# Performance work log

Measured on AMD Instinct MI355X. Metric: run time of the kernel, lower is better.

Reference implementation:

```python
import jax, jax.numpy as jnp
import numpy as np

# config: nsql-350M-like, 8 layers
L, D, H, HD, FF, V, RD, MP = 8, 1024, 16, 64, 4096, 51200, 32, 4


def setup_inputs() -> dict:
    key = jax.random.key(0)
    ks = jax.random.split(key, 8)
    B, S = 1, 1024
    s = 0.02
    return {
        'idx': jax.random.randint(ks[0], (B, S), 0, V),
        'input_pos': jnp.arange(S),
        'emb': jax.random.normal(ks[1], (V, D)) * s,
        'Wqkv': jax.random.normal(ks[2], (L, 3 * D, D)) * s,
        'Wo': jax.random.normal(ks[3], (L, D, D)) * s,
        'ln1_w': jnp.ones((L, D)), 'ln1_b': jnp.zeros((L, D)),
        'fc_in_w': jax.random.normal(ks[4], (L, FF, D)) * s,
        'fc_in_b': jnp.zeros((L, FF)),
        'fc_out_w': jax.random.normal(ks[5], (L, D, FF)) * s,
        'fc_out_b': jnp.zeros((L, D)),
        'lnf_w': jnp.ones((D,)), 'lnf_b': jnp.zeros((D,)),
        'lm_w': jax.random.normal(ks[6], (V, D)) * s,
        'lm_b': jnp.zeros((V,)),
    }


def _layer_norm(x, w, b, eps=1e-5):
    mu = jnp.mean(x, axis=-1, keepdims=True)
    var = jnp.var(x, axis=-1, keepdims=True)
    return (x - mu) * jax.lax.rsqrt(var + eps) * w + b


def _new_gelu(x):
    # transformers NewGELUActivation == tanh-approx gelu
    return jax.nn.gelu(x, approximate=True)


def _sincos(input_pos):
    # create_sinusoidal_positions over rotary_dim, gathered at input_pos
    inv_freq = 1.0 / (10000.0 ** (jnp.arange(0, RD, 2, dtype=jnp.float32) / RD))
    ang = input_pos.astype(jnp.float32)[:, None] * inv_freq          # [S, RD/2]
    # repeat_interleave(..., 2, dim=-1) -> interleaved sin/cos, shape [1,S,1,RD]
    sin = jnp.repeat(jnp.sin(ang), 2, axis=-1)[None, :, None, :]
    cos = jnp.repeat(jnp.cos(ang), 2, axis=-1)[None, :, None, :]
    return sin, cos


def _rotary(x, sin, cos):
    # x: [B,S,H,HD]; GPT-J interleaved rotary on first RD dims
    xr, xp = x[..., :RD], x[..., RD:]
    x1, x2 = xr[..., ::2], xr[..., 1::2]
    rot = jnp.stack((-x2, x1), axis=-1).reshape(xr.shape)  # rotate_every_two
    return jnp.concatenate([xr * cos + rot * sin, xp], axis=-1)


def reference(idx, input_pos, emb, Wqkv, Wo, ln1_w, ln1_b, fc_in_w, fc_in_b,
              fc_out_w, fc_out_b, lnf_w, lnf_b, lm_w, lm_b):
    B, S = idx.shape
    x = emb[idx]                                        # [B,S,D]
    sin, cos = _sincos(input_pos)
    causal = jnp.tril(jnp.ones((S, S), dtype=bool))
    neg = jnp.finfo(x.dtype).min
    ld = D // MP

    def split_heads(t):
        # CodeGen _split_heads with mp_num=4: [B,S,MP,ld] -> [B,S,H,HD]
        return t.reshape(B, S, MP, H // MP, HD).reshape(B, S, H, HD)

    for l in range(L):
        h = _layer_norm(x, ln1_w[l], ln1_b[l])
        qkv = (h @ Wqkv[l].T).reshape(B, S, MP, 3 * ld)
        q, v, k = qkv[..., :ld], qkv[..., ld:2 * ld], qkv[..., 2 * ld:]  # q,v,k order!
        q = _rotary(split_heads(q), sin, cos)
        k = _rotary(split_heads(k), sin, cos)
        vh = split_heads(v)
        q, k, vh = (jnp.transpose(t, (0, 2, 1, 3)) for t in (q, k, vh))  # [B,H,S,HD]
        scores = jnp.einsum('bhqd,bhkd->bhqk', q, k) / jnp.sqrt(jnp.asarray(HD, x.dtype))
        scores = jnp.where(causal, scores, neg)
        att = jax.nn.softmax(scores, axis=-1)
        y = jnp.einsum('bhqk,bhkd->bhqd', att, vh)
        y = jnp.transpose(y, (0, 2, 1, 3)).reshape(B, S, D)
        attn_out = y @ Wo[l].T
        mlp = _new_gelu(h @ fc_in_w[l].T + fc_in_b[l]) @ fc_out_w[l].T + fc_out_b[l]
        x = attn_out + mlp + x                          # parallel block + residual

    x = _layer_norm(x, lnf_w, lnf_b)
    return x @ lm_w.T + lm_b                            # [B,S,V]
```

## Files before the change

kernel.cpp:

```cpp
#include <hip/hip_runtime.h>

#define SQ 1024
#define DIM 1024
#define NH 16
#define HDIM 64
#define FFD 4096
#define NV 51200
#define NL 8
#define LDBUF 5120

typedef __bf16 bf16x8 __attribute__((ext_vector_type(8)));
typedef float f32x4 __attribute__((ext_vector_type(4)));

__device__ __forceinline__ unsigned short f2bf(float f) {
    union { float f; unsigned int i; } v; v.f = f;
    unsigned int r = v.i + 0x7fffu + ((v.i >> 16) & 1u);
    return (unsigned short)(r >> 16);
}
__device__ __forceinline__ float gelu_tanh(float x) {
    float x3 = x * x * x;
    return 0.5f * x * (1.0f + tanhf(0.79788456080286535588f * (x + 0.044715f * x3)));
}

#define GLD16(gp, lp) __builtin_amdgcn_global_load_lds( \
    (__attribute__((address_space(1))) void*)(gp), \
    (__attribute__((address_space(3))) void*)(lp), 16, 0, 0)
#define VMCNT0 asm volatile("s_waitcnt vmcnt(0)" ::: "memory")

__global__ void cvt4_kernel(const float* __restrict__ w0, const float* __restrict__ w1,
                            const float* __restrict__ w2, const float* __restrict__ w3,
                            unsigned short* __restrict__ d0, unsigned short* __restrict__ d1,
                            unsigned short* __restrict__ d2, unsigned short* __restrict__ d3) {
    const int b = blockIdx.x;
    const float* s; unsigned short* d; long off;
    if (b < 1536)      { s = w0; d = d0; off = (long)b * 2048; }
    else if (b < 2048) { s = w1; d = d1; off = (long)(b - 1536) * 2048; }
    else if (b < 4096) { s = w2; d = d2; off = (long)(b - 2048) * 2048; }
    else               { s = w3; d = d3; off = (long)(b - 4096) * 2048; }
    const long i = off + threadIdx.x * 8;
    float4 a = *reinterpret_cast<const float4*>(s + i);
    float4 c = *reinterpret_cast<const float4*>(s + i + 4);
    bf16x8 w;
    w[0] = (__bf16)a.x; w[1] = (__bf16)a.y; w[2] = (__bf16)a.z; w[3] = (__bf16)a.w;
    w[4] = (__bf16)c.x; w[5] = (__bf16)c.y; w[6] = (__bf16)c.z; w[7] = (__bf16)c.w;
    *reinterpret_cast<bf16x8*>(d + i) = w;
}
__global__ void cvt_kernel(const float* __restrict__ src, unsigned short* __restrict__ dst) {
    const long i = ((long)blockIdx.x * 256 + threadIdx.x) * 8;
    float4 a = *reinterpret_cast<const float4*>(src + i);
    float4 b = *reinterpret_cast<const float4*>(src + i + 4);
    bf16x8 w;
    w[0] = (__bf16)a.x; w[1] = (__bf16)a.y; w[2] = (__bf16)a.z; w[3] = (__bf16)a.w;
    w[4] = (__bf16)b.x; w[5] = (__bf16)b.y; w[6] = (__bf16)b.z; w[7] = (__bf16)b.w;
    *reinterpret_cast<bf16x8*>(dst + i) = w;
}

__global__ void sincos_kernel(const int* __restrict__ pos, float2* __restrict__ sc) {
    const int t = blockIdx.x * 256 + threadIdx.x;
    if (t >= SQ * 16) return;
    const int s = t >> 4, i = t & 15;
    const float ang = (float)pos[s] * powf(10000.0f, -(float)i / 16.0f);
    sc[t] = make_float2(sinf(ang), cosf(ang));
}

__global__ void embed_kernel(const int* __restrict__ idx, const float* __restrict__ emb,
                             float* __restrict__ x) {
    const int s = blockIdx.x;
    const int d = threadIdx.x * 4;
    const int row = idx[s];
    *reinterpret_cast<float4*>(x + (long)s * DIM + d) =
        *reinterpret_cast<const float4*>(emb + (long)row * DIM + d);
}

template <bool RED>
__global__ __launch_bounds__(256) void ln_kernel(float* __restrict__ x,
                                                 const float* __restrict__ part,
                                                 const float* __restrict__ w,
                                                 const float* __restrict__ b,
                                                 unsigned short* __restrict__ out) {
    __shared__ float red[8];
    const int s = blockIdx.x, tid = threadIdx.x;
    const long fidx = (long)s * 256 + tid;
    float4 v = reinterpret_cast<const float4*>(x)[fidx];
    if (RED) {
        #pragma unroll
        for (int z = 0; z < 8; z++) {
            float4 p = reinterpret_cast<const float4*>(part + (long)z * SQ * DIM)[fidx];
            v.x += p.x; v.y += p.y; v.z += p.z; v.w += p.w;
        }
        reinterpret_cast<float4*>(x)[fidx] = v;
    }
    float sum = v.x + v.y + v.z + v.w;
    float sq = v.x * v.x + v.y * v.y + v.z * v.z + v.w * v.w;
    #pragma unroll
    for (int off = 32; off; off >>= 1) { sum += __shfl_xor(sum, off); sq += __shfl_xor(sq, off); }
    const int wid = tid >> 6, lane = tid & 63;
    if (lane == 0) { red[wid * 2] = sum; red[wid * 2 + 1] = sq; }
    __syncthreads();
    sum = red[0] + red[2] + red[4] + red[6];
    sq  = red[1] + red[3] + red[5] + red[7];
    const float mu = sum * (1.0f / DIM);
    const float var = sq * (1.0f / DIM) - mu * mu;
    const float rstd = rsqrtf(var + 1e-5f);
    const int d = tid * 4;
    float vv[4] = {v.x, v.y, v.z, v.w};
    ushort4 o;
    unsigned short* op = (unsigned short*)&o;
    #pragma unroll
    for (int j = 0; j < 4; j++)
        op[j] = f2bf((vv[j] - mu) * rstd * w[d + j] + b[d + j]);
    *reinterpret_cast<ushort4*>(out + (long)s * DIM + d) = o;
}

__global__ __launch_bounds__(256) void gemm_qkv_fcin(const unsigned short* __restrict__ A,
                                                     const unsigned short* __restrict__ B1,
                                                     const unsigned short* __restrict__ B2,
                                                     const float* __restrict__ bias,
                                                     unsigned short* __restrict__ ffout,
                                                     const float2* __restrict__ sc,
                                                     unsigned short* __restrict__ qt,
                                                     unsigned short* __restrict__ kt,
                                                     unsigned short* __restrict__ vt) {
    __shared__ __align__(16) unsigned short As[2][128 * 64];
    __shared__ __align__(16) unsigned short Bs[2][128 * 64];
    const int tid = threadIdx.x;
    const int nwg = gridDim.x, qch = nwg >> 3;
    const int sb = (blockIdx.x & 7) * qch + (blockIdx.x >> 3);
    const int mb = sb & 7, nb = sb >> 3;
    const int m0 = mb * 128, n0 = nb * 128;
    const int lane = tid & 63, wid = tid >> 6;
    const int l15 = lane & 15, lhi = lane >> 4;
    const int wr = wid >> 1, wc = wid & 1;
    const int sw = l15 & 7;

    const unsigned short* Bbase = B1;
    int nloc = n0;
    if (nb >= 24) { Bbase = B2; nloc = n0 - 3072; }

    f32x4 acc[4][4];
    #pragma unroll
    for (int i = 0; i < 4; i++)
        #pragma unroll
        for (int j = 0; j < 4; j++) acc[i][j] = (f32x4){0.f, 0.f, 0.f, 0.f};

    const int wbase = (tid & ~63) * 8;

    auto stage = [&](int buf, int kt_) {
        const int k0 = kt_ << 6;
        #pragma unroll
        for (int i = 0; i < 4; i++) {
            const int e = (i * 256 + tid) * 8;
            const int r = e >> 6;
            const int cs = (((e >> 3) & 7) ^ (r & 7)) * 8;
            GLD16(A + (long)(m0 + r) * DIM + k0 + cs, &As[buf][i * 2048 + wbase]);
        }
        #pragma unroll
        for (int i = 0; i < 4; i++) {
            const int e = (i * 256 + tid) * 8;
            const int r = e >> 6;
            const int cs = (((e >> 3) & 7) ^ (r & 7)) * 8;
            GLD16(Bbase + (long)(nloc + r) * 1024 + k0 + cs, &Bs[buf][i * 2048 + wbase]);
        }
    };
    auto compute = [&](int buf) {
        #pragma unroll
        for (int ks = 0; ks < 2; ks++) {
            bf16x8 af[4], bfr[4];
            #pragma unroll
            for (int mf = 0; mf < 4; mf++)
                af[mf] = *reinterpret_cast<const bf16x8*>(
                    &As[buf][(wr * 64 + mf * 16 + l15) * 64 + ((ks * 4 + lhi) ^ sw) * 8]);
            #pragma unroll
            for (int nf = 0; nf < 4; nf++)
                bfr[nf] = *reinterpret_cast<const bf16x8*>(
                    &Bs[buf][(wc * 64 + nf * 16 + l15) * 64 + ((ks * 4 + lhi) ^ sw) * 8]);
            #pragma unroll
            for (int mf = 0; mf < 4; mf++)
                #pragma unroll
                for (int nf = 0; nf < 4; nf++)
                    acc[mf][nf] = __builtin_amdgcn_mfma_f32_16x16x32_bf16(af[mf], bfr[nf], acc[mf][nf], 0, 0, 0);
        }
    };

    int cur = 0;
    stage(0, 0);
    VMCNT0; __syncthreads();
    for (int kt_ = 0; kt_ < 16; kt_++) {
        if (kt_ + 1 < 16) stage(cur ^ 1, kt_ + 1);
        compute(cur);
        if (kt_ + 1 < 16) { VMCNT0; __syncthreads(); cur ^= 1; }
    }

    if (nb < 24) {
        #pragma unroll
        for (int nf = 0; nf < 4; nf++) {
            const int col = n0 + wc * 64 + nf * 16 + l15;
            const int g = col / 768;
            const int r768 = col - g * 768;
            const int sec = r768 >> 8;
            const int off = r768 & 255;
            const int h = g * 4 + (off >> 6);
            const int d = off & 63;
            const bool isrot = (d < 32);
            const int dodd = d & 1;
            #pragma unroll
            for (int mf = 0; mf < 4; mf++) {
                #pragma unroll
                for (int j = 0; j < 4; j++) {
                    const int row = m0 + wr * 64 + mf * 16 + lhi * 4 + j;
                    float v = acc[mf][nf][j];
                    const float pv = __shfl_xor(v, 1);
                    float outv = v;
                    if (isrot && sec != 1) {
                        const float2 scv = sc[row * 16 + (d >> 1)];
                        outv = dodd ? (v * scv.y + pv * scv.x)
                                    : (v * scv.y - pv * scv.x);
                    }
                    if (sec == 0)      qt[((long)(h * SQ + row)) * HDIM + d] = f2bf(outv);
                    else if (sec == 2) kt[((long)(h * SQ + row)) * HDIM + d] = f2bf(outv);
                    else               vt[(long)h * (HDIM * SQ) + (long)d * SQ + row] = f2bf(outv);
                }
            }
        }
    } else {
        #pragma unroll
        for (int nf = 0; nf < 4; nf++) {
            const int col = n0 + wc * 64 + nf * 16 + l15;
            #pragma unroll
            for (int mf = 0; mf < 4; mf++) {
                #pragma unroll
                for (int j = 0; j < 4; j++) {
                    const int row = m0 + wr * 64 + mf * 16 + lhi * 4 + j;
                    float v = gelu_tanh(acc[mf][nf][j] + bias[col - 3072]);
                    ffout[(long)row * LDBUF + (col - 3072)] = f2bf(v);
                }
            }
        }
    }
}

__global__ __launch_bounds__(256) void attn_fcout(const unsigned short* __restrict__ qt,
                                                  const unsigned short* __restrict__ kt,
                                                  const unsigned short* __restrict__ vt,
                                                  unsigned short* __restrict__ buf,
                                                  const unsigned short* __restrict__ fcw,
                                                  const float* __restrict__ fcb,
                                                  float* __restrict__ parts) {
    __shared__ __align__(16) unsigned short smem[32768];
    const int tid = threadIdx.x, lane = tid & 63, wid = tid >> 6;
    const int l15 = lane & 15, lhi = lane >> 4;
    const int sw = l15 & 7;
    const int wbase = (tid & ~63) * 8;

    if (blockIdx.x < 256) {
        unsigned short* Ks0 = smem;
        unsigned short* Vs0 = smem + 8192;
        unsigned short* Psw = smem + 16384 + wid * 1024;
        const int h = blockIdx.x & 15;
        const int qb = 15 - ((int)blockIdx.x >> 4);
        const int q0 = qb * 64 + wid * 16;

        bf16x8 aq[2];
        {
            const unsigned short* qp = qt + ((long)(h * SQ + q0 + l15)) * HDIM;
            aq[0] = *reinterpret_cast<const bf16x8*>(qp + lhi * 8);
            aq[1] = *reinterpret_cast<const bf16x8*>(qp + 32 + lhi * 8);
        }
        f32x4 o[4];
        #pragma unroll
        for (int nf = 0; nf < 4; nf++) o[nf] = (f32x4){0.f, 0.f, 0.f, 0.f};
        float mrow[4] = {-1e30f, -1e30f, -1e30f, -1e30f};
        float lrow[4] = {0.f, 0.f, 0.f, 0.f};

        auto stageKV = [&](int b, int kv0) {
            #pragma unroll
            for (int i = 0; i < 2; i++) {
                const int e = (i * 256 + tid) * 8;
                const int r = e >> 6;
                const int cs = (((e >> 3) & 7) ^ (r & 7)) * 8;
                GLD16(kt + ((long)(h * SQ + kv0 + r)) * HDIM + cs, Ks0 + b * 4096 + i * 2048 + wbase);
                GLD16(vt + (long)h * (HDIM * SQ) + (long)r * SQ + kv0 + cs, Vs0 + b * 4096 + i * 2048 + wbase);
            }
        };

        int cur = 0;
        stageKV(0, 0);
        VMCNT0; __syncthreads();
        for (int kvt = 0; kvt <= qb; kvt++) {
            const int kv0 = kvt * 64;
            if (kvt < qb) stageKV(cur ^ 1, kv0 + 64);

            f32x4 sa[4];
            #pragma unroll
            for (int hc = 0; hc < 4; hc++) sa[hc] = (f32x4){0.f, 0.f, 0.f, 0.f};
            #pragma unroll
            for (int hc = 0; hc < 4; hc++)
                #pragma unroll
                for (int ks = 0; ks < 2; ks++) {
                    bf16x8 bk = *reinterpret_cast<const bf16x8*>(
                        Ks0 + cur * 4096 + (hc * 16 + l15) * 64 + ((ks * 4 + lhi) ^ sw) * 8);
                    sa[hc] = __builtin_amdgcn_mfma_f32_16x16x32_bf16(aq[ks], bk, sa[hc], 0, 0, 0);
                }
            float pr[4][4], mb[4];
            #pragma unroll
            for (int j = 0; j < 4; j++) {
                const int qi = q0 + lhi * 4 + j;
                #pragma unroll
                for (int hc = 0; hc < 4; hc++) {
                    const int ki = kv0 + hc * 16 + l15;
                    const float sv = sa[hc][j] * 0.125f;
                    pr[hc][j] = (ki <= qi) ? sv : -1e30f;
                }
                mb[j] = fmaxf(fmaxf(pr[0][j], pr[1][j]), fmaxf(pr[2][j], pr[3][j]));
            }
            #pragma unroll
            for (int off = 1; off < 16; off <<= 1)
                #pragma unroll
                for (int j = 0; j < 4; j++) mb[j] = fmaxf(mb[j], __shfl_xor(mb[j], off));
            float alpha[4], psum[4];
            #pragma unroll
            for (int j = 0; j < 4; j++) {
                const float mn = fmaxf(mrow[j], mb[j]);
                alpha[j] = __expf(mrow[j] - mn);
                mrow[j] = mn;
                psum[j] = 0.f;
                #pragma unroll
                for (int hc = 0; hc < 4; hc++) { pr[hc][j] = __expf(pr[hc][j] - mn); psum[j] += pr[hc][j]; }
            }
            #pragma unroll
            for (int off = 1; off < 16; off <<= 1)
                #pragma unroll
                for (int j = 0; j < 4; j++) psum[j] += __shfl_xor(psum[j], off);
            #pragma unroll
            for (int j = 0; j < 4; j++) lrow[j] = lrow[j] * alpha[j] + psum[j];
            #pragma unroll
            for (int nf = 0; nf < 4; nf++)
                #pragma unroll
                for (int j = 0; j < 4; j++) o[nf][j] *= alpha[j];
            #pragma unroll
            for (int hc = 0; hc < 4; hc++)
                #pragma unroll
                for (int j = 0; j < 4; j++) {
                    const int prow = lhi * 4 + j;
                    const int pc8 = (hc * 2 + (l15 >> 3)) ^ (prow & 7);
                    Psw[prow * 64 + pc8 * 8 + (l15 & 7)] = f2bf(pr[hc][j]);
                }
            bf16x8 ap[2];
            ap[0] = *reinterpret_cast<const bf16x8*>(Psw + l15 * 64 + ((0 + lhi) ^ sw) * 8);
            ap[1] = *reinterpret_cast<const bf16x8*>(Psw + l15 * 64 + ((4 + lhi) ^ sw) * 8);
            #pragma unroll
            for (int nf = 0; nf < 4; nf++)
                #pragma unroll
                for (int ks2 = 0; ks2 < 2; ks2++) {
                    bf16x8 bv = *reinterpret_cast<const bf16x8*>(
                        Vs0 + cur * 4096 + (nf * 16 + l15) * 64 + ((ks2 * 4 + lhi) ^ sw) * 8);
                    o[nf] = __builtin_amdgcn_mfma_f32_16x16x32_bf16(ap[ks2], bv, o[nf], 0, 0, 0);
                }
            if (kvt < qb) { VMCNT0; __syncthreads(); cur ^= 1; }
        }
        #pragma unroll
        for (int nf = 0; nf < 4; nf++)
            #pragma unroll
            for (int j = 0; j < 4; j++) {
                const int row = q0 + lhi * 4 + j;
                buf[(long)row * LDBUF + h * HDIM + nf * 16 + l15] = f2bf(o[nf][j] / lrow[j]);
            }
    } else {
        unsigned short* As0 = smem;
        unsigned short* Bs0 = smem + 16384;
        const int b2 = (int)blockIdx.x - 256;
        const int sb = (b2 & 7) * 64 + (b2 >> 3);
        const int kz = sb & 7, nb = (sb >> 3) & 7, mb = sb >> 6;
        const int m0 = mb * 128, n0 = nb * 128;
        const int kt0 = kz * 8;
        const int wr = wid >> 1, wc = wid & 1;
        const unsigned short* Aff = buf + DIM;

        f32x4 acc[4][4];
        #pragma unroll
        for (int i = 0; i < 4; i++)
            #pragma unroll
            for (int j = 0; j < 4; j++) acc[i][j] = (f32x4){0.f, 0.f, 0.f, 0.f};

        auto stage = [&](int bf_, int kt_) {
            const int k0 = kt_ << 6;
            #pragma unroll
            for (int i = 0; i < 4; i++) {
                const int e = (i * 256 + tid) * 8;
                const int r = e >> 6;
                const int cs = (((e >> 3) & 7) ^ (r & 7)) * 8;
                GLD16(Aff + (long)(m0 + r) * LDBUF + k0 + cs, As0 + bf_ * 8192 + i * 2048 + wbase);
                GLD16(fcw + (long)(n0 + r) * FFD + k0 + cs, Bs0 + bf_ * 8192 + i * 2048 + wbase);
            }
        };
        auto compute = [&](int bf_) {
            #pragma unroll
            for (int ks = 0; ks < 2; ks++) {
                bf16x8 af[4], bfr[4];
                #pragma unroll
                for (int mf = 0; mf < 4; mf++)
                    af[mf] = *reinterpret_cast<const bf16x8*>(
                        As0 + bf_ * 8192 + (wr * 64 + mf * 16 + l15) * 64 + ((ks * 4 + lhi) ^ sw) * 8);
                #pragma unroll
                for (int nf = 0; nf < 4; nf++)
                    bfr[nf] = *reinterpret_cast<const bf16x8*>(
                        Bs0 + bf_ * 8192 + (wc * 64 + nf * 16 + l15) * 64 + ((ks * 4 + lhi) ^ sw) * 8);
                #pragma unroll
                for (int mf = 0; mf < 4; mf++)
                    #pragma unroll
                    for (int nf = 0; nf < 4; nf++)
                        acc[mf][nf] = __builtin_amdgcn_mfma_f32_16x16x32_bf16(af[mf], bfr[nf], acc[mf][nf], 0, 0, 0);
            }
        };

        int cur = 0;
        stage(0, kt0);
        VMCNT0; __syncthreads();
        for (int t = 0; t < 8; t++) {
            if (t + 1 < 8) stage(cur ^ 1, kt0 + t + 1);
            compute(cur);
            if (t + 1 < 8) { VMCNT0; __syncthreads(); cur ^= 1; }
        }

        float* P = parts + (long)kz * SQ * DIM;
        #pragma unroll
        for (int nf = 0; nf < 4; nf++) {
            const int col = n0 + wc * 64 + nf * 16 + l15;
            const float bv = (kz == 0) ? fcb[col] : 0.f;
            #pragma unroll
            for (int mf = 0; mf < 4; mf++) {
                #pragma unroll
                for (int j = 0; j < 4; j++) {
                    const int row = m0 + wr * 64 + mf * 16 + lhi * 4 + j;
                    P[(long)row * DIM + col] = acc[mf][nf][j] + bv;
                }
            }
        }
    }
}

__global__ __launch_bounds__(256) void wo_rmw(const unsigned short* __restrict__ buf,
                                              const unsigned short* __restrict__ wo,
                                              float* __restrict__ parts) {
    __shared__ __align__(16) unsigned short As[2][128 * 64];
    __shared__ __align__(16) unsigned short Bs[2][128 * 64];
    const int tid = threadIdx.x;
    const int sb = (blockIdx.x & 7) * 32 + (blockIdx.x >> 3);
    const int kz = sb & 3, nb = (sb >> 2) & 7, mb = sb >> 5;
    const int m0 = mb * 128, n0 = nb * 128;
    const int kt0 = kz * 4;
    const int lane = tid & 63, wid = tid >> 6;
    const int l15 = lane & 15, lhi = lane >> 4;
    const int wr = wid >> 1, wc = wid & 1;
    const int sw = l15 & 7;
    const int wbase = (tid & ~63) * 8;

    f32x4 acc[4][4];
    #pragma unroll
    for (int i = 0; i < 4; i++)
        #pragma unroll
        for (int j = 0; j < 4; j++) acc[i][j] = (f32x4){0.f, 0.f, 0.f, 0.f};

    auto stage = [&](int bf_, int kt_) {
        const int k0 = kt_ << 6;
        #pragma unroll
        for (int i = 0; i < 4; i++) {
            const int e = (i * 256 + tid) * 8;
            const int r = e >> 6;
            const int cs = (((e >> 3) & 7) ^ (r & 7)) * 8;
            GLD16(buf + (long)(m0 + r) * LDBUF + k0 + cs, &As[bf_][i * 2048 + wbase]);
            GLD16(wo + (long)(n0 + r) * DIM + k0 + cs, &Bs[bf_][i * 2048 + wbase]);
        }
    };
    auto compute = [&](int bf_) {
        #pragma unroll
        for (int ks = 0; ks < 2; ks++) {
            bf16x8 af[4], bfr[4];
            #pragma unroll
            for (int mf = 0; mf < 4; mf++)
                af[mf] = *reinterpret_cast<const bf16x8*>(
                    &As[bf_][(wr * 64 + mf * 16 + l15) * 64 + ((ks * 4 + lhi) ^ sw) * 8]);
            #pragma unroll
            for (int nf = 0; nf < 4; nf++)
                bfr[nf] = *reinterpret_cast<const bf16x8*>(
                    &Bs[bf_][(wc * 64 + nf * 16 + l15) * 64 + ((ks * 4 + lhi) ^ sw) * 8]);
            #pragma unroll
            for (int mf = 0; mf < 4; mf++)
                #pragma unroll
                for (int nf = 0; nf < 4; nf++)
                    acc[mf][nf] = __builtin_amdgcn_mfma_f32_16x16x32_bf16(af[mf], bfr[nf], acc[mf][nf], 0, 0, 0);
        }
    };

    int cur = 0;
    stage(0, kt0);
    VMCNT0; __syncthreads();
    for (int t = 0; t < 4; t++) {
        if (t + 1 < 4) stage(cur ^ 1, kt0 + t + 1);
        compute(cur);
        if (t + 1 < 4) { VMCNT0; __syncthreads(); cur ^= 1; }
    }

    float* P = parts + (long)kz * SQ * DIM;
    #pragma unroll
    for (int nf = 0; nf < 4; nf++) {
        const int col = n0 + wc * 64 + nf * 16 + l15;
        #pragma unroll
        for (int mf = 0; mf < 4; mf++) {
            #pragma unroll
            for (int j = 0; j < 4; j++) {
                const int row = m0 + wr * 64 + mf * 16 + lhi * 4 + j;
                const long idx = (long)row * DIM + col;
                P[idx] += acc[mf][nf][j];
            }
        }
    }
}

__global__ __launch_bounds__(512) void gemm256(const unsigned short* __restrict__ A,
                                               const unsigned short* __restrict__ B,
                                               const float* __restrict__ bias,
                                               float* __restrict__ C) {
    __shared__ __align__(16) unsigned short As[2][256 * 64];
    __shared__ __align__(16) unsigned short Bs[2][256 * 64];
    const int tid = threadIdx.x;
    const int nwg = gridDim.x, qch = nwg >> 3;
    const int sb = (blockIdx.x & 7) * qch + (blockIdx.x >> 3);
    const int mb = sb & 3, nb = sb >> 2;
    const int m0 = mb * 256, n0 = nb * 256;
    const int lane = tid & 63, wid = tid >> 6;
    const int l15 = lane & 15, lhi = lane >> 4;
    const int wm = wid >> 2, wn = wid & 3;
    const int sw = l15 & 7;

    f32x4 acc[8][4];
    #pragma unroll
    for (int i = 0; i < 8; i++)
        #pragma unroll
        for (int j = 0; j < 4; j++) acc[i][j] = (f32x4){0.f, 0.f, 0.f, 0.f};

    const int wbase = (tid & ~63) * 8;

    auto stage = [&](int buf, int kt) {
        const int k0 = kt << 6;
        #pragma unroll
        for (int i = 0; i < 4; i++) {
            const int e = (i * 512 + tid) * 8;
            const int r = e >> 6;
            const int cs = (((e >> 3) & 7) ^ (r & 7)) * 8;
            GLD16(A + (long)(m0 + r) * 1024 + k0 + cs, &As[buf][i * 4096 + wbase]);
            GLD16(B + (long)(n0 + r) * 1024 + k0 + cs, &Bs[buf][i * 4096 + wbase]);
        }
    };
    auto compute = [&](int buf) {
        #pragma unroll
        for (int ks = 0; ks < 2; ks++) {
            bf16x8 af[8], bfr[4];
            #pragma unroll
            for (int mf = 0; mf < 8; mf++)
                af[mf] = *reinterpret_cast<const bf16x8*>(
                    &As[buf][(wm * 128 + mf * 16 + l15) * 64 + ((ks * 4 + lhi) ^ sw) * 8]);
            #pragma unroll
            for (int nf = 0; nf < 4; nf++)
                bfr[nf] = *reinterpret_cast<const bf16x8*>(
                    &Bs[buf][(wn * 64 + nf * 16 + l15) * 64 + ((ks * 4 + lhi) ^ sw) * 8]);
            #pragma unroll
            for (int mf = 0; mf < 8; mf++)
                #pragma unroll
                for (int nf = 0; nf < 4; nf++)
                    acc[mf][nf] = __builtin_amdgcn_mfma_f32_16x16x32_bf16(af[mf], bfr[nf], acc[mf][nf], 0, 0, 0);
        }
    };

    int cur = 0;
    stage(0, 0);
    VMCNT0; __syncthreads();
    for (int kt = 0; kt < 16; kt++) {
        if (kt < 15) stage(cur ^ 1, kt + 1);
        compute(cur);
        if (kt < 15) { VMCNT0; __syncthreads(); cur ^= 1; }
    }

    #pragma unroll
    for (int nf = 0; nf < 4; nf++) {
        const int col = n0 + wn * 64 + nf * 16 + l15;
        const float bv = bias[col];
        #pragma unroll
        for (int mf = 0; mf < 8; mf++) {
            #pragma unroll
            for (int j = 0; j < 4; j++) {
                const int row = m0 + wm * 128 + mf * 16 + lhi * 4 + j;
                C[(long)row * NV + col] = acc[mf][nf][j] + bv;
            }
        }
    }
}

extern "C" void kernel_launch(void* const* d_in, const int* in_sizes, int n_in,
                              void* d_out, int out_size, void* d_ws, size_t ws_size,
                              hipStream_t stream) {
    const int* idx    = (const int*)d_in[0];
    const int* pos    = (const int*)d_in[1];
    const float* emb  = (const float*)d_in[2];
    const float* Wqkv = (const float*)d_in[3];
    const float* Wo   = (const float*)d_in[4];
    const float* ln1w = (const float*)d_in[5];
    const float* ln1b = (const float*)d_in[6];
    const float* fciw = (const float*)d_in[7];
    const float* fcib = (const float*)d_in[8];
    const float* fcow = (const float*)d_in[9];
    const float* fcob = (const float*)d_in[10];
    const float* lnfw = (const float*)d_in[11];
    const float* lnfb = (const float*)d_in[12];
    const float* lmw  = (const float*)d_in[13];
    const float* lmb  = (const float*)d_in[14];

    char* ws = (char*)d_ws;
    unsigned short* wbuf = (unsigned short*)ws;   ws += (long)NV * DIM * 2;
    unsigned short* wqkvb = wbuf;
    unsigned short* wob   = wbuf + (long)3072 * 1024;
    unsigned short* fcinb = wob + (long)1024 * 1024;
    unsigned short* fcoutb= fcinb + (long)4096 * 1024;
    float* x           = (float*)ws;          ws += (long)SQ * DIM * 4;
    float* parts       = (float*)ws;          ws += (long)8 * SQ * DIM * 4;
    unsigned short* h  = (unsigned short*)ws; ws += (long)SQ * DIM * 2;
    unsigned short* qt = (unsigned short*)ws; ws += (long)NH * SQ * HDIM * 2;
    unsigned short* kt = (unsigned short*)ws; ws += (long)NH * SQ * HDIM * 2;
    unsigned short* vt = (unsigned short*)ws; ws += (long)NH * SQ * HDIM * 2;
    unsigned short* buf= (unsigned short*)ws; ws += (long)SQ * LDBUF * 2;
    float2* sc         = (float2*)ws;         ws += (long)SQ * 16 * 8;

    sincos_kernel<<<64, 256, 0, stream>>>(pos, sc);
    embed_kernel<<<SQ, 256, 0, stream>>>(idx, emb, x);

    for (int l = 0; l < NL; l++) {
        cvt4_kernel<<<6144, 256, 0, stream>>>(Wqkv + (long)l * 3 * DIM * DIM,
                                              Wo   + (long)l * DIM * DIM,
                                              fciw + (long)l * FFD * DIM,
                                              fcow + (long)l * DIM * FFD,
                                              wqkvb, wob, fcinb, fcoutb);

        if (l == 0) ln_kernel<false><<<SQ, 256, 0, stream>>>(x, nullptr, ln1w, ln1b, h);
        else ln_kernel<true><<<SQ, 256, 0, stream>>>(x, parts, ln1w + (long)l * DIM, ln1b + (long)l * DIM, h);

        gemm_qkv_fcin<<<448, 256, 0, stream>>>(h, wqkvb, fcinb, fcib + (long)l * FFD,
                                               buf + DIM, sc, qt, kt, vt);
        attn_fcout<<<768, 256, 0, stream>>>(qt, kt, vt, buf, fcoutb, fcob + (long)l * DIM, parts);
        wo_rmw<<<256, 256, 0, stream>>>(buf, wob, parts);
    }
    cvt_kernel<<<25600, 256, 0, stream>>>(lmw, wbuf);
    ln_kernel<true><<<SQ, 256, 0, stream>>>(x, parts, lnfw, lnfb, h);
    gemm256<<<800, 512, 0, stream>>>(h, wbuf, lmb, (float*)d_out);
}
```

Before: 1.094 ms.

## Overlap next-layer weight conversion with attention/fc-out via double-buffered weights

Per-layer fp32-to-bf16 weight conversion and the final LM-head conversion are moved into 512 extra blocks of the attn_fcout launch. These blocks convert the next layer's weights into an alternate buffer and one eighth of the LM weights each layer. The aim is to hide the conversion memory traffic behind attention and fc-out compute and to remove separate launches. It needs a larger workspace and falls back to the old path when the workspace is too small. The extra blocks compete with attention and GEMM blocks for bandwidth and CU slots.

```diff
diff --git a/kernel.cpp b/kernel.cpp
--- a/kernel.cpp
+++ b/kernel.cpp
@@ -8,6 +8,7 @@
 #define NV 51200
 #define NL 8
 #define LDBUF 5120
+#define WELEMS ((long)(3 * DIM + DIM + FFD + FFD) * DIM)
 
 typedef __bf16 bf16x8 __attribute__((ext_vector_type(8)));
 typedef float f32x4 __attribute__((ext_vector_type(4)));
@@ -21,6 +22,14 @@
     float x3 = x * x * x;
     return 0.5f * x * (1.0f + tanhf(0.79788456080286535588f * (x + 0.044715f * x3)));
 }
+__device__ __forceinline__ void cvt8(const float* __restrict__ s, unsigned short* __restrict__ d, long i) {
+    float4 a = *reinterpret_cast<const float4*>(s + i);
+    float4 b = *reinterpret_cast<const float4*>(s + i + 4);
+    bf16x8 w;
+    w[0] = (__bf16)a.x; w[1] = (__bf16)a.y; w[2] = (__bf16)a.z; w[3] = (__bf16)a.w;
+    w[4] = (__bf16)b.x; w[5] = (__bf16)b.y; w[6] = (__bf16)b.z; w[7] = (__bf16)b.w;
+    *reinterpret_cast<bf16x8*>(d + i) = w;
+}
 
 #define GLD16(gp, lp) __builtin_amdgcn_global_load_lds( \
     (__attribute__((address_space(1))) void*)(gp), \
@@ -29,30 +38,17 @@
 
 __global__ void cvt4_kernel(const float* __restrict__ w0, const float* __restrict__ w1,
                             const float* __restrict__ w2, const float* __restrict__ w3,
-                            unsigned short* __restrict__ d0, unsigned short* __restrict__ d1,
-                            unsigned short* __restrict__ d2, unsigned short* __restrict__ d3) {
+                            unsigned short* __restrict__ dst) {
     const int b = blockIdx.x;
-    const float* s; unsigned short* d; long off;
-    if (b < 1536)      { s = w0; d = d0; off = (long)b * 2048; }
-    else if (b < 2048) { s = w1; d = d1; off = (long)(b - 1536) * 2048; }
-    else if (b < 4096) { s = w2; d = d2; off = (long)(b - 2048) * 2048; }
-    else               { s = w3; d = d3; off = (long)(b - 4096) * 2048; }
-    const long i = off + threadIdx.x * 8;
-    float4 a = *reinterpret_cast<const float4*>(s + i);
-    float4 c = *reinterpret_cast<const float4*>(s + i + 4);
-    bf16x8 w;
-    w[0] = (__bf16)a.x; w[1] = (__bf16)a.y; w[2] = (__bf16)a.z; w[3] = (__bf16)a.w;
-    w[4] = (__bf16)c.x; w[5] = (__bf16)c.y; w[6] = (__bf16)c.z; w[7] = (__bf16)c.w;
-    *reinterpret_cast<bf16x8*>(d + i) = w;
+    const float* s; long off; unsigned short* d;
+    if (b < 1536)      { s = w0; d = dst;                      off = (long)b * 2048; }
+    else if (b < 2048) { s = w1; d = dst + (long)3072 * 1024;  off = (long)(b - 1536) * 2048; }
+    else if (b < 4096) { s = w2; d = dst + (long)4096 * 1024;  off = (long)(b - 2048) * 2048; }
+    else               { s = w3; d = dst + (long)8192 * 1024;  off = (long)(b - 4096) * 2048; }
+    cvt8(s, d, off + threadIdx.x * 8);
 }
 __global__ void cvt_kernel(const float* __restrict__ src, unsigned short* __restrict__ dst) {
-    const long i = ((long)blockIdx.x * 256 + threadIdx.x) * 8;
-    float4 a = *reinterpret_cast<const float4*>(src + i);
-    float4 b = *reinterpret_cast<const float4*>(src + i + 4);
-    bf16x8 w;
-    w[0] = (__bf16)a.x; w[1] = (__bf16)a.y; w[2] = (__bf16)a.z; w[3] = (__bf16)a.w;
-    w[4] = (__bf16)b.x; w[5] = (__bf16)b.y; w[6] = (__bf16)b.z; w[7] = (__bf16)b.w;
-    *reinterpret_cast<bf16x8*>(dst + i) = w;
+    cvt8(src, dst, ((long)blockIdx.x * 256 + threadIdx.x) * 8);
 }
 
 __global__ void sincos_kernel(const int* __restrict__ pos, float2* __restrict__ sc) {
@@ -245,7 +241,14 @@
                                                   unsigned short* __restrict__ buf,
                                                   const unsigned short* __restrict__ fcw,
                                                   const float* __restrict__ fcb,
-                                                  float* __restrict__ parts) {
+                                                  float* __restrict__ parts,
+                                                  const float* __restrict__ nw0,
+                                                  const float* __restrict__ nw1,
+                                                  const float* __restrict__ nw2,
+                                                  const float* __restrict__ nw3,
+                                                  unsigned short* __restrict__ nd,
+                                                  const float* __restrict__ lmsrc,
+                                                  unsigned short* __restrict__ lmdst) {
     __shared__ __align__(16) unsigned short smem[32768];
     const int tid = threadIdx.x, lane = tid & 63, wid = tid >> 6;
     const int l15 = lane & 15, lhi = lane >> 4;
@@ -365,7 +368,7 @@
                 const int row = q0 + lhi * 4 + j;
                 buf[(long)row * LDBUF + h * HDIM + nf * 16 + l15] = f2bf(o[nf][j] / lrow[j]);
             }
-    } else {
+    } else if (blockIdx.x < 768) {
         unsigned short* As0 = smem;
         unsigned short* Bs0 = smem + 16384;
         const int b2 = (int)blockIdx.x - 256;
@@ -435,6 +438,26 @@
                     P[(long)row * DIM + col] = acc[mf][nf][j] + bv;
                 }
             }
+        }
+    } else {
+        const int cb = (int)blockIdx.x - 768;
+        const int nch = (int)gridDim.x - 768;
+        const long stride = (long)nch * 256;
+        const long base = (long)cb * 256 + tid;
+        if (nd) {
+            const long n0v = (long)3072 * 1024 / 8, n1v = (long)1024 * 1024 / 8;
+            const long n2v = (long)4096 * 1024 / 8, n3v = (long)4096 * 1024 / 8;
+            for (long i = base; i < n0v; i += stride) cvt8(nw0, nd, i * 8);
+            unsigned short* d1 = nd + n0v * 8;
+            for (long i = base; i < n1v; i += stride) cvt8(nw1, d1, i * 8);
+            unsigned short* d2 = d1 + n1v * 8;
+            for (long i = base; i < n2v; i += stride) cvt8(nw2, d2, i * 8);
+            unsigned short* d3 = d2 + n2v * 8;
+            for (long i = base; i < n3v; i += stride) cvt8(nw3, d3, i * 8);
+        }
+        if (lmdst) {
+            const long nlmv = (long)(NV / NL) * DIM / 8;
+            for (long i = base; i < nlmv; i += stride) cvt8(lmsrc, lmdst, i * 8);
         }
     }
 }
@@ -510,8 +533,7 @@
             #pragma unroll
             for (int j = 0; j < 4; j++) {
                 const int row = m0 + wr * 64 + mf * 16 + lhi * 4 + j;
-                const long idx = (long)row * DIM + col;
-                P[idx] += acc[mf][nf][j];
+                P[(long)row * DIM + col] += acc[mf][nf][j];
             }
         }
     }
@@ -615,12 +637,22 @@
     const float* lmw  = (const float*)d_in[13];
     const float* lmb  = (const float*)d_in[14];
 
+    const long tailBytes = (long)SQ * DIM * 4 + (long)8 * SQ * DIM * 4 + (long)SQ * DIM * 2
+                         + (long)3 * NH * SQ * HDIM * 2 + (long)SQ * LDBUF * 2 + (long)SQ * 16 * 8;
+    const long bigBytes  = 2 * WELEMS * 2 + (long)NV * DIM * 2 + tailBytes;
+    const bool big = (long)ws_size >= bigBytes + (1 << 20);
+
     char* ws = (char*)d_ws;
-    unsigned short* wbuf = (unsigned short*)ws;   ws += (long)NV * DIM * 2;
-    unsigned short* wqkvb = wbuf;
-    unsigned short* wob   = wbuf + (long)3072 * 1024;
-    unsigned short* fcinb = wob + (long)1024 * 1024;
-    unsigned short* fcoutb= fcinb + (long)4096 * 1024;
+    unsigned short *wbufA, *wbufB, *lmbuf;
+    if (big) {
+        wbufA = (unsigned short*)ws; ws += WELEMS * 2;
+        wbufB = (unsigned short*)ws; ws += WELEMS * 2;
+        lmbuf = (unsigned short*)ws; ws += (long)NV * DIM * 2;
+    } else {
+        wbufA = (unsigned short*)ws; ws += (long)NV * DIM * 2;
+        wbufB = wbufA;
+        lmbuf = wbufA;
+    }
     float* x           = (float*)ws;          ws += (long)SQ * DIM * 4;
     float* parts       = (float*)ws;          ws += (long)8 * SQ * DIM * 4;
     unsigned short* h  = (unsigned short*)ws; ws += (long)SQ * DIM * 2;
@@ -630,25 +662,51 @@
     unsigned short* buf= (unsigned short*)ws; ws += (long)SQ * LDBUF * 2;
     float2* sc         = (float2*)ws;         ws += (long)SQ * 16 * 8;
 
+    auto wq = [&](unsigned short* wb) { return wb; };
+    auto wo_ = [&](unsigned short* wb) { return wb + (long)3072 * 1024; };
+    auto wfi = [&](unsigned short* wb) { return wb + (long)4096 * 1024; };
+    auto wfo = [&](unsigned short* wb) { return wb + (long)8192 * 1024; };
+
     sincos_kernel<<<64, 256, 0, stream>>>(pos, sc);
     embed_kernel<<<SQ, 256, 0, stream>>>(idx, emb, x);
+    cvt4_kernel<<<6144, 256, 0, stream>>>(Wqkv, Wo, fciw, fcow, wbufA);
 
     for (int l = 0; l < NL; l++) {
-        cvt4_kernel<<<6144, 256, 0, stream>>>(Wqkv + (long)l * 3 * DIM * DIM,
-                                              Wo   + (long)l * DIM * DIM,
-                                              fciw + (long)l * FFD * DIM,
-                                              fcow + (long)l * DIM * FFD,
-                                              wqkvb, wob, fcinb, fcoutb);
+        unsigned short* wb = (l & 1) ? wbufB : wbufA;
+        unsigned short* wn = (l & 1) ? wbufA : wbufB;
+
+        if (!big && l > 0)
+            cvt4_kernel<<<6144, 256, 0, stream>>>(Wqkv + (long)l * 3 * DIM * DIM,
+                                                  Wo   + (long)l * DIM * DIM,
+                                                  fciw + (long)l * FFD * DIM,
+                                                  fcow + (long)l * DIM * FFD, wb);
 
         if (l == 0) ln_kernel<false><<<SQ, 256, 0, stream>>>(x, nullptr, ln1w, ln1b, h);
         else ln_kernel<true><<<SQ, 256, 0, stream>>>(x, parts, ln1w + (long)l * DIM, ln1b + (long)l * DIM, h);
 
-        gemm_qkv_fcin<<<448, 256, 0, stream>>>(h, wqkvb, fcinb, fcib + (long)l * FFD,
+        gemm_qkv_fcin<<<448, 256, 0, stream>>>(h, wq(wb), wfi(wb), fcib + (long)l * FFD,
                                                buf + DIM, sc, qt, kt, vt);
-        attn_fcout<<<768, 256, 0, stream>>>(qt, kt, vt, buf, fcoutb, fcob + (long)l * DIM, parts);
-        wo_rmw<<<256, 256, 0, stream>>>(buf, wob, parts);
-    }
-    cvt_kernel<<<25600, 256, 0, stream>>>(lmw, wbuf);
+        if (big) {
+            const int nl = l + 1;
+            const float* n0 = (nl < NL) ? Wqkv + (long)nl * 3 * DIM * DIM : nullptr;
+            const float* n1 = (nl < NL) ? Wo   + (long)nl * DIM * DIM : nullptr;
+            const float* n2 = (nl < NL) ? fciw + (long)nl * FFD * DIM : nullptr;
+            const float* n3 = (nl < NL) ? fcow + (long)nl * DIM * FFD : nullptr;
+            unsigned short* ndst = (nl < NL) ? wn : nullptr;
+            attn_fcout<<<768 + 512, 256, 0, stream>>>(qt, kt, vt, buf, wfo(wb),
+                                                      fcob + (long)l * DIM, parts,
+                                                      n0, n1, n2, n3, ndst,
+                                                      lmw + (long)l * (NV / NL) * DIM,
+                                                      lmbuf + (long)l * (NV / NL) * DIM);
+        } else {
+            attn_fcout<<<768, 256, 0, stream>>>(qt, kt, vt, buf, wfo(wb),
+                                                fcob + (long)l * DIM, parts,
+                                                nullptr, nullptr, nullptr, nullptr, nullptr,
+                                                nullptr, nullptr);
+        }
+        wo_rmw<<<256, 256, 0, stream>>>(buf, wo_(wb), parts);
+    }
+    if (!big) cvt_kernel<<<25600, 256, 0, stream>>>(lmw, lmbuf);
     ln_kernel<true><<<SQ, 256, 0, stream>>>(x, parts, lnfw, lnfb, h);
-    gemm256<<<800, 512, 0, stream>>>(h, wbuf, lmb, (float*)d_out);
-}
+    gemm256<<<800, 512, 0, stream>>>(h, lmbuf, lmb, (float*)d_out);
+}
```

Measured after the change: 1.030 ms. -5.9%, faster.
